# Performance work log

Hardware: AMD Instinct MI355X
Metric: run time of the kernel (lower is better)

The kernel has to match this reference:

```python
import jax, jax.numpy as jnp
import numpy as np

N_SRC = 50000
N_DST = 50000
N_EDGES = 600000
IN_FEAT = 128
OUT_FEAT = 128


def setup_inputs() -> dict:
    key = jax.random.key(0)
    k1, k2, k3, k4, k5, k6 = jax.random.split(key, 6)
    h_s = jax.random.normal(k1, (N_SRC, IN_FEAT), dtype=jnp.float32)
    h_d = jax.random.normal(k2, (N_DST, IN_FEAT), dtype=jnp.float32)
    src = jax.random.randint(k3, (N_EDGES,), 0, N_SRC, dtype=jnp.int32)
    dst = jax.random.randint(k4, (N_EDGES,), 0, N_DST, dtype=jnp.int32)
    # nn.Linear(in_feat*2, out_feat): W [out, 2*in], b [out]
    W = jax.random.normal(k5, (OUT_FEAT, 2 * IN_FEAT), dtype=jnp.float32) * 0.05
    b = jax.random.normal(k6, (OUT_FEAT,), dtype=jnp.float32) * 0.05
    return {"h_s": h_s, "h_d": h_d, "src": src, "dst": dst, "W": W, "b": b}


def reference(h_s, h_d, src, dst, W, b):
    # copy_u + mean: gather source features along edges, segment-mean by dst
    msgs = h_s[src]  # [E, in_feat]
    neigh_sum = jax.ops.segment_sum(msgs, dst, num_segments=N_DST)  # [n_dst, in_feat]
    deg = jax.ops.segment_sum(jnp.ones((src.shape[0],), dtype=h_s.dtype), dst,
                              num_segments=N_DST)
    h_neigh = neigh_sum / jnp.maximum(deg, 1.0)[:, None]  # zero-degree -> 0
    # concat + linear (dropout is identity in eval mode)
    feat = jnp.concatenate([h_d, h_neigh], axis=1)  # [n_dst, 2*in_feat]
    out = feat @ W.T + b  # [n_dst, out_feat]
    return out
```

## Files before the change

kernel.cpp:

```cpp
#include <hip/hip_runtime.h>
#include <hip/hip_bf16.h>

#define N_SRC 50000
#define N_DST 50000
#define N_EDGES 600000
#define IN_FEAT 128
#define OUT_FEAT 128
#define CAP 64

typedef __attribute__((ext_vector_type(8))) short short8;
typedef __attribute__((ext_vector_type(4))) float float4v;
typedef __attribute__((ext_vector_type(4))) float f32x4;

#define FILL_BLOCKS ((N_EDGES + 255) / 256)
#define HS4 (N_SRC * IN_FEAT / 4)
#define CVT_BLOCKS (HS4 / 256)
#define W_BLOCKS 16
#define K1_GRID (FILL_BLOCKS + 2 * CVT_BLOCKS + W_BLOCKS)

__global__ __launch_bounds__(256) void fill_cvt_kernel(
    const float* __restrict__ h_s, const float* __restrict__ h_d,
    const float* __restrict__ W,
    const int* __restrict__ src, const int* __restrict__ dst,
    int* __restrict__ deg, ushort* __restrict__ permu,
    ushort* __restrict__ hsb, ushort* __restrict__ hdb,
    ushort* __restrict__ wfrag)
{
    int bid = blockIdx.x;
    int tid = threadIdx.x;

    if (bid < FILL_BLOCKS) {
        int e = bid * 256 + tid;
        if (e < N_EDGES) {
            int s = __builtin_nontemporal_load(src + e);
            int d = __builtin_nontemporal_load(dst + e);
            int p = atomicAdd(&deg[d], 1);
            if (p < CAP) permu[(size_t)d * CAP + p] = (ushort)s;
        }
        return;
    }
    bid -= FILL_BLOCKS;

    if (bid < 2 * CVT_BLOCKS) {
        bool first = (bid < CVT_BLOCKS);
        const float* in = first ? h_s : h_d;
        ushort* outp    = first ? hsb : hdb;
        int idx = (first ? bid : bid - CVT_BLOCKS) * 256 + tid;
        f32x4 v = __builtin_nontemporal_load((const f32x4*)in + idx);
        __hip_bfloat16 o[4];
        o[0] = __float2bfloat16(v.x);
        o[1] = __float2bfloat16(v.y);
        o[2] = __float2bfloat16(v.z);
        o[3] = __float2bfloat16(v.w);
        *(ushort4*)(outp + (size_t)idx * 4) = *(ushort4*)o;
        return;
    }
    bid -= 2 * CVT_BLOCKS;

    int c = bid * 256 + tid;
    int f  = c >> 6;
    int l  = c & 63;
    int ks = f >> 3;
    int nt = f & 7;
    int row = nt * 16 + (l & 15);
    int col = ks * 32 + (l >> 4) * 8;
    const float* wp = W + (size_t)row * 256 + col;
    f32x4 w0 = __builtin_nontemporal_load((const f32x4*)wp);
    f32x4 w1 = __builtin_nontemporal_load((const f32x4*)wp + 1);
    __hip_bfloat16 o[8];
    o[0] = __float2bfloat16(w0.x); o[1] = __float2bfloat16(w0.y);
    o[2] = __float2bfloat16(w0.z); o[3] = __float2bfloat16(w0.w);
    o[4] = __float2bfloat16(w1.x); o[5] = __float2bfloat16(w1.y);
    o[6] = __float2bfloat16(w1.z); o[7] = __float2bfloat16(w1.w);
    *(short8*)(wfrag + (size_t)c * 8) = *(short8*)o;
}

__global__ __launch_bounds__(256) void gather_kernel(
    const ushort* __restrict__ hsb, const int* __restrict__ deg,
    const ushort* __restrict__ permu, ushort* __restrict__ neighb)
{
    int wave = threadIdx.x >> 6;
    int lane = threadIdx.x & 63;
    int row  = blockIdx.x * 4 + wave;
    if (row >= N_DST) return;

    int dg  = deg[row];
    int dgr = (dg < CAP) ? dg : CAP;
    const ushort* prow = permu + (size_t)row * CAP;
    int s0 = (dgr > 0) ? (int)prow[0] : 0;

    float ax = 0.f, ay = 0.f;
    for (int j = 0; j < dgr; j += 8) {
        ushort4 pa = *(const ushort4*)(prow + j);
        ushort4 pb = *(const ushort4*)(prow + j + 4);
        int t[8] = {pa.x, pa.y, pa.z, pa.w, pb.x, pb.y, pb.z, pb.w};
        int   s[8];
        float m[8];
#pragma unroll
        for (int q = 0; q < 8; ++q) {
            bool ok = (j + q < dgr);
            s[q] = ok ? t[q] : s0;
            m[q] = ok ? 1.f : 0.f;
        }
        ushort2 u[8];
#pragma unroll
        for (int q = 0; q < 8; ++q)
            u[q] = ((const ushort2*)(hsb + (size_t)s[q] * IN_FEAT))[lane];
#pragma unroll
        for (int q = 0; q < 8; ++q) {
            ax += m[q] * __uint_as_float((unsigned)u[q].x << 16);
            ay += m[q] * __uint_as_float((unsigned)u[q].y << 16);
        }
    }
    float inv = (dg > 0) ? (1.0f / (float)dg) : 0.0f;
    __hip_bfloat16 ox = __float2bfloat16(ax * inv);
    __hip_bfloat16 oy = __float2bfloat16(ay * inv);
    ushort2 o = make_ushort2(*(ushort*)&ox, *(ushort*)&oy);
    ((ushort2*)(neighb + (size_t)row * IN_FEAT))[lane] = o;
}

__global__ __launch_bounds__(256) void gemm_mfma_kernel(
    const ushort* __restrict__ hdb, const ushort* __restrict__ neighb,
    const ushort* __restrict__ wfrag, const float* __restrict__ b,
    float* __restrict__ out)
{
    __shared__ ushort sWb[64 * 64 * 8];

    int tid  = threadIdx.x;
    int wave = tid >> 6;
    int lane = tid & 63;
    int lm   = lane & 15;
    int lk   = (lane >> 4) * 8;

#pragma unroll
    for (int i = 0; i < 16; ++i) {
        int c = i * 256 + tid;
        *(short8*)(sWb + (size_t)c * 8) = *(const short8*)(wfrag + (size_t)c * 8);
    }
    __syncthreads();

    int row0 = blockIdx.x * 128 + wave * 32;

    float4v acc0[8], acc1[8];
#pragma unroll
    for (int nt = 0; nt < 8; ++nt) {
        acc0[nt] = (float4v){0.f, 0.f, 0.f, 0.f};
        acc1[nt] = (float4v){0.f, 0.f, 0.f, 0.f};
    }

    int ar0 = row0 + lm;       ar0 = (ar0 < N_DST) ? ar0 : (N_DST - 1);
    int ar1 = row0 + 16 + lm;  ar1 = (ar1 < N_DST) ? ar1 : (N_DST - 1);
    const ushort* a0h = hdb    + (size_t)ar0 * IN_FEAT + lk;
    const ushort* a1h = hdb    + (size_t)ar1 * IN_FEAT + lk;
    const ushort* a0n = neighb + (size_t)ar0 * IN_FEAT + lk;
    const ushort* a1n = neighb + (size_t)ar1 * IN_FEAT + lk;

#pragma unroll
    for (int ks = 0; ks < 8; ++ks) {
        int koff = (ks & 3) * 32;
        short8 af0 = (ks < 4) ? *(const short8*)(a0h + koff)
                              : *(const short8*)(a0n + koff);
        short8 af1 = (ks < 4) ? *(const short8*)(a1h + koff)
                              : *(const short8*)(a1n + koff);
#pragma unroll
        for (int nt = 0; nt < 8; ++nt) {
            short8 bf = *(const short8*)(sWb + ((size_t)(ks * 8 + nt) * 64 + lane) * 8);
            acc0[nt] = __builtin_amdgcn_mfma_f32_16x16x32_bf16(af0, bf, acc0[nt], 0, 0, 0);
            acc1[nt] = __builtin_amdgcn_mfma_f32_16x16x32_bf16(af1, bf, acc1[nt], 0, 0, 0);
        }
    }

    int orow0 = row0 + (lane >> 4) * 4;
#pragma unroll
    for (int nt = 0; nt < 8; ++nt) {
        int col = nt * 16 + lm;
        float bias = b[col];
#pragma unroll
        for (int r = 0; r < 4; ++r) {
            int oa = orow0 + r;
            int ob = oa + 16;
            if (oa < N_DST) out[(size_t)oa * OUT_FEAT + col] = acc0[nt][r] + bias;
            if (ob < N_DST) out[(size_t)ob * OUT_FEAT + col] = acc1[nt][r] + bias;
        }
    }
}

extern "C" void kernel_launch(void* const* d_in, const int* in_sizes, int n_in,
                              void* d_out, int out_size, void* d_ws, size_t ws_size,
                              hipStream_t stream) {
    const float* h_s = (const float*)d_in[0];
    const float* h_d = (const float*)d_in[1];
    const int*   src = (const int*)d_in[2];
    const int*   dst = (const int*)d_in[3];
    const float* W   = (const float*)d_in[4];
    const float* b   = (const float*)d_in[5];
    float* out = (float*)d_out;

    char* ws = (char*)d_ws;
    int*    deg    = (int*)ws;
    ushort* permu  = (ushort*)(ws + 200000);
    ushort* hsb    = (ushort*)(ws + 6600000);
    ushort* hdb    = (ushort*)(ws + 19400000);
    ushort* neighb = (ushort*)(ws + 32200000);
    ushort* wfrag  = (ushort*)(ws + 45000000);

    hipMemsetAsync(deg, 0, N_DST * sizeof(int), stream);

    fill_cvt_kernel<<<K1_GRID, 256, 0, stream>>>(
        h_s, h_d, W, src, dst, deg, permu, hsb, hdb, wfrag);
    gather_kernel<<<(N_DST + 3) / 4, 256, 0, stream>>>(
        hsb, deg, permu, neighb);
    gemm_mfma_kernel<<<(N_DST + 127) / 128, 256, 0, stream>>>(
        hdb, neighb, wfrag, b, out);
}
```

Baseline: 180.0 us.

## Fuse neighbor gather into MFMA GEMM via swizzled LDS tile

Merges the gather/mean kernel and the GEMM kernel into one 512-thread kernel. Each block first gathers and averages 128 destination rows into an XOR-swizzled shared-memory tile, then runs the bf16 MFMA GEMM reading the neighbor half from LDS and W fragments directly from global memory instead of staging them in LDS. This removes the neighb round trip through HBM and one launch. In exchange there are only about 391 large blocks, and each wave processes 16 rows serially in the gather phase, which lowers parallelism for the latency-bound gather. Separately, the conversion kernel's nontemporal hints move from the input loads to the output stores.

```diff
diff --git a/kernel.cpp b/kernel.cpp
--- a/kernel.cpp
+++ b/kernel.cpp
@@ -11,6 +11,7 @@
 typedef __attribute__((ext_vector_type(8))) short short8;
 typedef __attribute__((ext_vector_type(4))) float float4v;
 typedef __attribute__((ext_vector_type(4))) float f32x4;
+typedef __attribute__((ext_vector_type(4))) unsigned short ushort4v;
 
 #define FILL_BLOCKS ((N_EDGES + 255) / 256)
 #define HS4 (N_SRC * IN_FEAT / 4)
@@ -46,13 +47,13 @@
         const float* in = first ? h_s : h_d;
         ushort* outp    = first ? hsb : hdb;
         int idx = (first ? bid : bid - CVT_BLOCKS) * 256 + tid;
-        f32x4 v = __builtin_nontemporal_load((const f32x4*)in + idx);
+        f32x4 v = *((const f32x4*)in + idx);
         __hip_bfloat16 o[4];
         o[0] = __float2bfloat16(v.x);
         o[1] = __float2bfloat16(v.y);
         o[2] = __float2bfloat16(v.z);
         o[3] = __float2bfloat16(v.w);
-        *(ushort4*)(outp + (size_t)idx * 4) = *(ushort4*)o;
+        __builtin_nontemporal_store(*(ushort4v*)o, (ushort4v*)(outp + (size_t)idx * 4));
         return;
     }
     bid -= 2 * CVT_BLOCKS;
@@ -65,122 +66,108 @@
     int row = nt * 16 + (l & 15);
     int col = ks * 32 + (l >> 4) * 8;
     const float* wp = W + (size_t)row * 256 + col;
-    f32x4 w0 = __builtin_nontemporal_load((const f32x4*)wp);
-    f32x4 w1 = __builtin_nontemporal_load((const f32x4*)wp + 1);
+    f32x4 w0 = *(const f32x4*)wp;
+    f32x4 w1 = *((const f32x4*)wp + 1);
     __hip_bfloat16 o[8];
     o[0] = __float2bfloat16(w0.x); o[1] = __float2bfloat16(w0.y);
     o[2] = __float2bfloat16(w0.z); o[3] = __float2bfloat16(w0.w);
     o[4] = __float2bfloat16(w1.x); o[5] = __float2bfloat16(w1.y);
     o[6] = __float2bfloat16(w1.z); o[7] = __float2bfloat16(w1.w);
-    *(short8*)(wfrag + (size_t)c * 8) = *(short8*)o;
+    __builtin_nontemporal_store(*(short8*)o, (short8*)(wfrag + (size_t)c * 8));
 }
 
-__global__ __launch_bounds__(256) void gather_kernel(
+__global__ __launch_bounds__(512) void gather_gemm_kernel(
     const ushort* __restrict__ hsb, const int* __restrict__ deg,
-    const ushort* __restrict__ permu, ushort* __restrict__ neighb)
-{
-    int wave = threadIdx.x >> 6;
-    int lane = threadIdx.x & 63;
-    int row  = blockIdx.x * 4 + wave;
-    if (row >= N_DST) return;
-
-    int dg  = deg[row];
-    int dgr = (dg < CAP) ? dg : CAP;
-    const ushort* prow = permu + (size_t)row * CAP;
-    int s0 = (dgr > 0) ? (int)prow[0] : 0;
-
-    float ax = 0.f, ay = 0.f;
-    for (int j = 0; j < dgr; j += 8) {
-        ushort4 pa = *(const ushort4*)(prow + j);
-        ushort4 pb = *(const ushort4*)(prow + j + 4);
-        int t[8] = {pa.x, pa.y, pa.z, pa.w, pb.x, pb.y, pb.z, pb.w};
-        int   s[8];
-        float m[8];
-#pragma unroll
-        for (int q = 0; q < 8; ++q) {
-            bool ok = (j + q < dgr);
-            s[q] = ok ? t[q] : s0;
-            m[q] = ok ? 1.f : 0.f;
-        }
-        ushort2 u[8];
-#pragma unroll
-        for (int q = 0; q < 8; ++q)
-            u[q] = ((const ushort2*)(hsb + (size_t)s[q] * IN_FEAT))[lane];
-#pragma unroll
-        for (int q = 0; q < 8; ++q) {
-            ax += m[q] * __uint_as_float((unsigned)u[q].x << 16);
-            ay += m[q] * __uint_as_float((unsigned)u[q].y << 16);
-        }
-    }
-    float inv = (dg > 0) ? (1.0f / (float)dg) : 0.0f;
-    __hip_bfloat16 ox = __float2bfloat16(ax * inv);
-    __hip_bfloat16 oy = __float2bfloat16(ay * inv);
-    ushort2 o = make_ushort2(*(ushort*)&ox, *(ushort*)&oy);
-    ((ushort2*)(neighb + (size_t)row * IN_FEAT))[lane] = o;
-}
-
-__global__ __launch_bounds__(256) void gemm_mfma_kernel(
-    const ushort* __restrict__ hdb, const ushort* __restrict__ neighb,
+    const ushort* __restrict__ permu, const ushort* __restrict__ hdb,
     const ushort* __restrict__ wfrag, const float* __restrict__ b,
     float* __restrict__ out)
 {
-    __shared__ ushort sWb[64 * 64 * 8];
+    __shared__ ushort sN[128 * 128];
 
     int tid  = threadIdx.x;
     int wave = tid >> 6;
     int lane = tid & 63;
-    int lm   = lane & 15;
-    int lk   = (lane >> 4) * 8;
+    int row0 = blockIdx.x * 128;
 
+    for (int r = 0; r < 16; ++r) {
+        int lrow = wave * 16 + r;
+        int row  = row0 + lrow;
+        float ax = 0.f, ay = 0.f;
+        if (row < N_DST) {
+            int dg  = deg[row];
+            int dgr = (dg < CAP) ? dg : CAP;
+            const ushort* prow = permu + (size_t)row * CAP;
+            int s0 = (dgr > 0) ? (int)prow[0] : 0;
+            for (int j = 0; j < dgr; j += 8) {
+                ushort4 pa = *(const ushort4*)(prow + j);
+                ushort4 pb = *(const ushort4*)(prow + j + 4);
+                int t[8] = {pa.x, pa.y, pa.z, pa.w, pb.x, pb.y, pb.z, pb.w};
+                int   s[8];
+                float m[8];
 #pragma unroll
-    for (int i = 0; i < 16; ++i) {
-        int c = i * 256 + tid;
-        *(short8*)(sWb + (size_t)c * 8) = *(const short8*)(wfrag + (size_t)c * 8);
+                for (int q = 0; q < 8; ++q) {
+                    bool ok = (j + q < dgr);
+                    s[q] = ok ? t[q] : s0;
+                    m[q] = ok ? 1.f : 0.f;
+                }
+                ushort2 u[8];
+#pragma unroll
+                for (int q = 0; q < 8; ++q)
+                    u[q] = ((const ushort2*)(hsb + (size_t)s[q] * IN_FEAT))[lane];
+#pragma unroll
+                for (int q = 0; q < 8; ++q) {
+                    ax += m[q] * __uint_as_float((unsigned)u[q].x << 16);
+                    ay += m[q] * __uint_as_float((unsigned)u[q].y << 16);
+                }
+            }
+            float inv = (dg > 0) ? (1.0f / (float)dg) : 0.0f;
+            ax *= inv; ay *= inv;
+        }
+        __hip_bfloat16 ox = __float2bfloat16(ax);
+        __hip_bfloat16 oy = __float2bfloat16(ay);
+        unsigned byte = ((unsigned)(lrow * 256 + lane * 4)) ^ (((unsigned)lrow & 7u) << 4);
+        *(ushort2*)((char*)sN + byte) = make_ushort2(*(ushort*)&ox, *(ushort*)&oy);
     }
     __syncthreads();
 
-    int row0 = blockIdx.x * 128 + wave * 32;
+    int lm = lane & 15;
+    int lk = (lane >> 4) * 8;
+    int lrowA = wave * 16 + lm;
 
-    float4v acc0[8], acc1[8];
+    int ar = row0 + lrowA;  ar = (ar < N_DST) ? ar : (N_DST - 1);
+    const ushort* ah = hdb + (size_t)ar * IN_FEAT + lk;
+
+    float4v acc[8];
 #pragma unroll
-    for (int nt = 0; nt < 8; ++nt) {
-        acc0[nt] = (float4v){0.f, 0.f, 0.f, 0.f};
-        acc1[nt] = (float4v){0.f, 0.f, 0.f, 0.f};
-    }
-
-    int ar0 = row0 + lm;       ar0 = (ar0 < N_DST) ? ar0 : (N_DST - 1);
-    int ar1 = row0 + 16 + lm;  ar1 = (ar1 < N_DST) ? ar1 : (N_DST - 1);
-    const ushort* a0h = hdb    + (size_t)ar0 * IN_FEAT + lk;
-    const ushort* a1h = hdb    + (size_t)ar1 * IN_FEAT + lk;
-    const ushort* a0n = neighb + (size_t)ar0 * IN_FEAT + lk;
-    const ushort* a1n = neighb + (size_t)ar1 * IN_FEAT + lk;
+    for (int nt = 0; nt < 8; ++nt) acc[nt] = (float4v){0.f, 0.f, 0.f, 0.f};
 
 #pragma unroll
     for (int ks = 0; ks < 8; ++ks) {
         int koff = (ks & 3) * 32;
-        short8 af0 = (ks < 4) ? *(const short8*)(a0h + koff)
-                              : *(const short8*)(a0n + koff);
-        short8 af1 = (ks < 4) ? *(const short8*)(a1h + koff)
-                              : *(const short8*)(a1n + koff);
+        short8 af;
+        if (ks < 4) {
+            af = *(const short8*)(ah + koff);
+        } else {
+            unsigned byte = ((unsigned)(lrowA * 256 + (lk + koff) * 2))
+                            ^ (((unsigned)lrowA & 7u) << 4);
+            af = *(const short8*)((char*)sN + byte);
+        }
 #pragma unroll
         for (int nt = 0; nt < 8; ++nt) {
-            short8 bf = *(const short8*)(sWb + ((size_t)(ks * 8 + nt) * 64 + lane) * 8);
-            acc0[nt] = __builtin_amdgcn_mfma_f32_16x16x32_bf16(af0, bf, acc0[nt], 0, 0, 0);
-            acc1[nt] = __builtin_amdgcn_mfma_f32_16x16x32_bf16(af1, bf, acc1[nt], 0, 0, 0);
+            short8 bf = *(const short8*)(wfrag + ((size_t)(ks * 8 + nt) * 64 + lane) * 8);
+            acc[nt] = __builtin_amdgcn_mfma_f32_16x16x32_bf16(af, bf, acc[nt], 0, 0, 0);
         }
     }
 
-    int orow0 = row0 + (lane >> 4) * 4;
+    int orow0 = row0 + wave * 16 + (lane >> 4) * 4;
 #pragma unroll
     for (int nt = 0; nt < 8; ++nt) {
         int col = nt * 16 + lm;
         float bias = b[col];
 #pragma unroll
         for (int r = 0; r < 4; ++r) {
-            int oa = orow0 + r;
-            int ob = oa + 16;
-            if (oa < N_DST) out[(size_t)oa * OUT_FEAT + col] = acc0[nt][r] + bias;
-            if (ob < N_DST) out[(size_t)ob * OUT_FEAT + col] = acc1[nt][r] + bias;
+            int o = orow0 + r;
+            if (o < N_DST) out[(size_t)o * OUT_FEAT + col] = acc[nt][r] + bias;
         }
     }
 }
@@ -201,15 +188,12 @@
     ushort* permu  = (ushort*)(ws + 200000);
     ushort* hsb    = (ushort*)(ws + 6600000);
     ushort* hdb    = (ushort*)(ws + 19400000);
-    ushort* neighb = (ushort*)(ws + 32200000);
-    ushort* wfrag  = (ushort*)(ws + 45000000);
+    ushort* wfrag  = (ushort*)(ws + 32200000);
 
     hipMemsetAsync(deg, 0, N_DST * sizeof(int), stream);
 
     fill_cvt_kernel<<<K1_GRID, 256, 0, stream>>>(
         h_s, h_d, W, src, dst, deg, permu, hsb, hdb, wfrag);
-    gather_kernel<<<(N_DST + 3) / 4, 256, 0, stream>>>(
-        hsb, deg, permu, neighb);
-    gemm_mfma_kernel<<<(N_DST + 127) / 128, 256, 0, stream>>>(
-        hdb, neighb, wfrag, b, out);
+    gather_gemm_kernel<<<(N_DST + 127) / 128, 512, 0, stream>>>(
+        hsb, deg, permu, hdb, wfrag, b, out);
 }
```

Result: slower. 192.9 us (+7.2%).
